# Optimization experiments

Hardware: AMD Instinct MI355X
Metric: run time of the kernel (lower is better)

The kernel has to match this reference:

```python
import jax, jax.numpy as jnp
import numpy as np

N = 50000          # nodes
E_RAND = 800000    # random edges (avg degree 16); self-loops appended per PyG GATConv default
IN = 128
HID = 32
HEADS = 4
OUT = 32
NEG_SLOPE = 0.2    # PyG GATConv default LeakyReLU slope


def setup_inputs() -> dict:
    key = jax.random.key(0)
    ks = jax.random.split(key, 8)
    x = jax.random.normal(ks[0], (N, IN), dtype=jnp.float32)
    src = jax.random.randint(ks[1], (E_RAND,), 0, N)
    dst = jax.random.randint(ks[2], (E_RAND,), 0, N)
    loops = jnp.arange(N)
    src = jnp.concatenate([src, loops])  # [E] with self-loops
    dst = jnp.concatenate([dst, loops])
    inp = {"x": x, "src": src, "dst": dst}
    layer_dims = [(IN, HID), (HID * HEADS, HID), (HID * HEADS, OUT)]
    for l, (din, c) in enumerate(layer_dims):
        k1, k2, k3 = jax.random.split(ks[3 + l], 3)
        s = 1.0 / np.sqrt(din)
        inp[f"W{l}"] = jax.random.uniform(k1, (HEADS * c, din), jnp.float32, -s, s)
        inp[f"asrc{l}"] = jax.random.uniform(k2, (HEADS, c), jnp.float32, -s, s)
        inp[f"adst{l}"] = jax.random.uniform(k3, (HEADS, c), jnp.float32, -s, s)
        inp[f"b{l}"] = jnp.zeros((HEADS * c,), jnp.float32)
    return inp


def _gat_conv(x, src, dst, W, a_src, a_dst, b):
    H, C = a_src.shape
    h = (x @ W.T).reshape(-1, H, C)                     # [N, H, C]
    al_s = jnp.einsum('nhc,hc->nh', h, a_src)           # node-level src score
    al_d = jnp.einsum('nhc,hc->nh', h, a_dst)           # node-level dst score
    e = jax.nn.leaky_relu(al_s[src] + al_d[dst], NEG_SLOPE)  # [E, H]
    # segment softmax over edges sharing the same destination node
    e_max = jax.ops.segment_max(e, dst, num_segments=N)
    e = jnp.exp(e - e_max[dst])
    denom = jax.ops.segment_sum(e, dst, num_segments=N)
    alpha = e / (denom[dst] + 1e-16)                    # [E, H]
    out = jax.ops.segment_sum(alpha[:, :, None] * h[src], dst, num_segments=N)  # [N, H, C]
    return out.reshape(-1, H * C) + b


def reference(x, src, dst, W0, asrc0, adst0, b0, W1, asrc1, adst1, b1, W2, asrc2, adst2, b2):
    params = [(W0, asrc0, adst0, b0), (W1, asrc1, adst1, b1), (W2, asrc2, adst2, b2)]
    h = x
    for i, (W, a_s, a_d, b) in enumerate(params):
        h = _gat_conv(h, src, dst, W, a_s, a_d, b)
        if i != len(params) - 1:
            h = jax.nn.elu(h)  # dropout p=0.5 is identity in eval mode
    return h
```

## Files before the change

### kernel.cpp

```cpp
#include <hip/hip_runtime.h>
#include <stdint.h>

typedef unsigned short ushort_t;
typedef unsigned int uint32;

typedef __attribute__((ext_vector_type(8))) short short8;
typedef __attribute__((ext_vector_type(4))) float floatx4;

#define NEG_SLOPE 0.2f

__device__ __forceinline__ ushort_t f2bf(float f) {
    union { float f; uint32 u; } v; v.f = f;
    uint32 u = v.u;
    uint32 r = (u + 0x7fffu + ((u >> 16) & 1u)) >> 16;
    return (ushort_t)r;
}
__device__ __forceinline__ float2 bf2x(uint32 u) {
    union { uint32 u; float f; } a, b;
    a.u = u << 16; b.u = u & 0xffff0000u;
    float2 r; r.x = a.f; r.y = b.f; return r;
}

__global__ void k_sniff(const uint32* __restrict__ x, int* __restrict__ flag) {
    __shared__ int sh[256];
    int t = threadIdx.x;
    int c = 0;
    for (int i = t; i < 1024; i += 256) {
        uint32 h = x[i] & 0xFFFFu;
        uint32 e = (h >> 7) & 0xFFu;
        if (h == 0u || (e >= 100u && e <= 140u)) c++;
    }
    sh[t] = c; __syncthreads();
    for (int off = 128; off >= 1; off >>= 1) {
        if (t < off) sh[t] += sh[t + off];
        __syncthreads();
    }
    if (t == 0) flag[0] = (sh[0] >= 512) ? 1 : 0;
}

__device__ __forceinline__ void gemm_body(int bid, int tid,
                                          const void* __restrict__ actv,
                                          const ushort_t* __restrict__ W,
                                          ushort_t* __restrict__ hb,
                                          float* __restrict__ als,
                                          float* __restrict__ ald,
                                          const ushort_t* __restrict__ asrcp,
                                          const ushort_t* __restrict__ adstp,
                                          int N, int layer0,
                                          const int* __restrict__ flag) {
    int wid = tid >> 6, lane = tid & 63;
    int n0 = (bid * 4 + wid) * 16;
    int mrow = lane & 15, quad = lane >> 4;
    int n = n0 + mrow;
    bool isf32 = (layer0 && !flag[0]);
    short8 a[4];
    if (n < N) {
        if (isf32) {
            const float* ar = (const float*)actv + (size_t)n * 128 + quad * 8;
            #pragma unroll
            for (int kt = 0; kt < 4; kt++) {
                float4 fa = *(const float4*)(ar + kt * 32);
                float4 fb = *(const float4*)(ar + kt * 32 + 4);
                short8 v;
                v[0] = (short)f2bf(fa.x); v[1] = (short)f2bf(fa.y);
                v[2] = (short)f2bf(fa.z); v[3] = (short)f2bf(fa.w);
                v[4] = (short)f2bf(fb.x); v[5] = (short)f2bf(fb.y);
                v[6] = (short)f2bf(fb.z); v[7] = (short)f2bf(fb.w);
                a[kt] = v;
            }
        } else {
            const ushort_t* ar = (const ushort_t*)actv + (size_t)n * 128 + quad * 8;
            #pragma unroll
            for (int kt = 0; kt < 4; kt++) a[kt] = *(const short8*)(ar + kt * 32);
        }
    } else {
        #pragma unroll
        for (int kt = 0; kt < 4; kt++) { short8 z = {0,0,0,0,0,0,0,0}; a[kt] = z; }
    }
    float ps[4], pd[4];
    #pragma unroll
    for (int t = 0; t < 8; t++) {
        if ((t & 1) == 0) {
            #pragma unroll
            for (int r = 0; r < 4; r++) { ps[r] = 0.f; pd[r] = 0.f; }
        }
        const ushort_t* wr = W + (size_t)(t * 16 + mrow) * 128 + quad * 8;
        floatx4 acc = {0.f, 0.f, 0.f, 0.f};
        #pragma unroll
        for (int kt = 0; kt < 4; kt++) {
            short8 b = *(const short8*)(wr + kt * 32);
            acc = __builtin_amdgcn_mfma_f32_16x16x32_bf16(a[kt], b, acc, 0, 0, 0);
        }
        int col = t * 16 + mrow;
        union { uint32 u; float f; } cs, cd;
        cs.u = ((uint32)asrcp[col]) << 16;
        cd.u = ((uint32)adstp[col]) << 16;
        #pragma unroll
        for (int r = 0; r < 4; r++) {
            int rn = n0 + quad * 4 + r;
            if (rn < N) hb[(size_t)rn * 128 + col] = f2bf(acc[r]);
            ps[r] += acc[r] * cs.f;
            pd[r] += acc[r] * cd.f;
        }
        if (t & 1) {
            #pragma unroll
            for (int off = 1; off <= 8; off <<= 1) {
                #pragma unroll
                for (int r = 0; r < 4; r++) {
                    ps[r] += __shfl_xor(ps[r], off);
                    pd[r] += __shfl_xor(pd[r], off);
                }
            }
            int h = t >> 1;
            if (mrow < 8) {
                int r = mrow & 3;
                float vs = r == 0 ? ps[0] : r == 1 ? ps[1] : r == 2 ? ps[2] : ps[3];
                float vd = r == 0 ? pd[0] : r == 1 ? pd[1] : r == 2 ? pd[2] : pd[3];
                int rn = n0 + quad * 4 + r;
                if (rn < N) {
                    float* dp = (mrow < 4) ? als : ald;
                    dp[(size_t)rn * 4 + h] = (mrow < 4) ? vs : vd;
                }
            }
        }
    }
}

__global__ __launch_bounds__(256) void k_gemm(const void* __restrict__ actv,
                                              const ushort_t* __restrict__ W,
                                              ushort_t* __restrict__ hb,
                                              float* __restrict__ als,
                                              float* __restrict__ ald,
                                              const ushort_t* __restrict__ asrcp,
                                              const ushort_t* __restrict__ adstp,
                                              int N, const int* __restrict__ flag) {
    gemm_body(blockIdx.x, threadIdx.x, actv, W, hb, als, ald, asrcp, adstp, N, 0, flag);
}

__global__ void k_f1(const void* W0, const void* W1, const void* W2,
                     const void* s0, const void* s1, const void* s2,
                     const void* a0, const void* a1, const void* a2,
                     const void* b0, const void* b1, const void* b2,
                     ushort_t* __restrict__ pblk, const int* __restrict__ flag,
                     const int* __restrict__ dst, int* __restrict__ cnt,
                     int* __restrict__ rank, int E) {
    if (blockIdx.x < 197) {
        int i = blockIdx.x * 256 + threadIdx.x;
        if (i >= 50304) return;
        const void* src; int off;
        if (i < 49152) {
            int seg = i / 16384; off = i % 16384;
            src = seg == 0 ? W0 : seg == 1 ? W1 : W2;
        } else if (i < 49536) {
            int j = i - 49152; int seg = j / 128; off = j % 128;
            src = seg == 0 ? s0 : seg == 1 ? s1 : s2;
        } else if (i < 49920) {
            int j = i - 49536; int seg = j / 128; off = j % 128;
            src = seg == 0 ? a0 : seg == 1 ? a1 : a2;
        } else {
            int j = i - 49920; int seg = j / 128; off = j % 128;
            src = seg == 0 ? b0 : seg == 1 ? b1 : b2;
        }
        if (flag[0]) pblk[i] = ((const ushort_t*)src)[off];
        else         pblk[i] = f2bf(((const float*)src)[off]);
    } else {
        int e0 = ((blockIdx.x - 197) * 256 + threadIdx.x) * 4;
        if (e0 + 3 < E) {
            int4 d4 = *(const int4*)(dst + e0);
            int r0 = atomicAdd(&cnt[d4.x], 1);
            int r1 = atomicAdd(&cnt[d4.y], 1);
            int r2 = atomicAdd(&cnt[d4.z], 1);
            int r3 = atomicAdd(&cnt[d4.w], 1);
            int4 r4 = {r0, r1, r2, r3};
            *(int4*)(rank + e0) = r4;
        } else {
            for (int e = e0; e < E; e++) rank[e] = atomicAdd(&cnt[dst[e]], 1);
        }
    }
}

__global__ __launch_bounds__(256) void k_f2(const int* __restrict__ cnt, int* __restrict__ ro,
                                            int* __restrict__ bsum, int n, int nb,
                                            const void* __restrict__ actv,
                                            const ushort_t* __restrict__ W,
                                            ushort_t* __restrict__ hb,
                                            float* __restrict__ als, float* __restrict__ ald,
                                            const ushort_t* __restrict__ asrcp,
                                            const ushort_t* __restrict__ adstp,
                                            int N, const int* __restrict__ flag) {
    if ((int)blockIdx.x < nb) {
        __shared__ int sd[256];
        int t = threadIdx.x;
        int base = blockIdx.x * 1024 + t * 4;
        int v0 = (base + 0 < n) ? cnt[base + 0] : 0;
        int v1 = (base + 1 < n) ? cnt[base + 1] : 0;
        int v2 = (base + 2 < n) ? cnt[base + 2] : 0;
        int v3 = (base + 3 < n) ? cnt[base + 3] : 0;
        int s = v0 + v1 + v2 + v3;
        sd[t] = s; __syncthreads();
        for (int off = 1; off < 256; off <<= 1) {
            int x = 0;
            if (t >= off) x = sd[t - off];
            __syncthreads();
            sd[t] += x;
            __syncthreads();
        }
        int run = sd[t] - s;
        run += v0; if (base + 0 < n) ro[base + 1] = run;
        run += v1; if (base + 1 < n) ro[base + 2] = run;
        run += v2; if (base + 2 < n) ro[base + 3] = run;
        run += v3; if (base + 3 < n) ro[base + 4] = run;
        if (t == 255) bsum[blockIdx.x] = sd[255];
    } else {
        gemm_body(blockIdx.x - nb, threadIdx.x, actv, W, hb, als, ald, asrcp, adstp, N, 1, flag);
    }
}

__global__ void k_scan_bc(int* __restrict__ ro, const int* __restrict__ bsum,
                          int n, int nb) {
    __shared__ int pre[256];
    int t = threadIdx.x;
    if (t == 0) {
        int acc = 0;
        for (int b = 0; b < nb; b++) { pre[b] = acc; acc += bsum[b]; }
    }
    __syncthreads();
    int i = blockIdx.x * 256 + t;
    if (i == 0) ro[0] = 0;
    if (i < n) ro[i + 1] += pre[i >> 10];
}

__global__ void k_scatter(const int* __restrict__ src, const int* __restrict__ dst,
                          const int* __restrict__ ro, const int* __restrict__ rank,
                          ushort_t* __restrict__ ssrc, int E) {
    int e0 = (blockIdx.x * 256 + threadIdx.x) * 4;
    if (e0 + 3 < E) {
        int4 d4 = *(const int4*)(dst + e0);
        int4 s4 = *(const int4*)(src + e0);
        int4 r4 = *(const int4*)(rank + e0);
        ssrc[ro[d4.x] + r4.x] = (ushort_t)s4.x;
        ssrc[ro[d4.y] + r4.y] = (ushort_t)s4.y;
        ssrc[ro[d4.z] + r4.z] = (ushort_t)s4.z;
        ssrc[ro[d4.w] + r4.w] = (ushort_t)s4.w;
    } else {
        for (int e = e0; e < E; e++) ssrc[ro[dst[e]] + rank[e]] = (ushort_t)src[e];
    }
}

__global__ __launch_bounds__(64) void k_agg(const int* __restrict__ ro,
                                            const ushort_t* __restrict__ ssrc,
                                            const ushort_t* __restrict__ hb,
                                            const float* __restrict__ als,
                                            const float* __restrict__ ald_,
                                            const ushort_t* __restrict__ bias,
                                            void* __restrict__ outp, int N, int apply_elu,
                                            int is_final, const int* __restrict__ flag) {
    int n = blockIdx.x;
    int lane = threadIdx.x;
    int r0 = ro[n], r1 = ro[n + 1];
    floatx4 ad = *(const floatx4*)(ald_ + (size_t)n * 4);
    const char* alsb = (const char*)als;

    __shared__ __align__(16) float wsm[256];
    __shared__ int osm[64];
    float a0 = 0.f, a1 = 0.f;
    float d0 = 0.f, d1 = 0.f, d2 = 0.f, d3 = 0.f;
    int hd = lane >> 4;
    int laneb = lane << 2;
    for (int base = r0; base < r1; base += 64) {
        int i = base + lane;
        if (i < r1) {
            int s = ssrc[i];
            floatx4 as = *(const floatx4*)(alsb + (s << 4));
            float t0 = as.x + ad.x; float w0 = __expf(fmaxf(t0, NEG_SLOPE * t0)); d0 += w0;
            float t1 = as.y + ad.y; float w1 = __expf(fmaxf(t1, NEG_SLOPE * t1)); d1 += w1;
            float t2 = as.z + ad.z; float w2 = __expf(fmaxf(t2, NEG_SLOPE * t2)); d2 += w2;
            float t3 = as.w + ad.w; float w3 = __expf(fmaxf(t3, NEG_SLOPE * t3)); d3 += w3;
            osm[lane] = s << 8;
            floatx4 w4 = {w0, w1, w2, w3};
            *(floatx4*)(wsm + lane * 4) = w4;
        }
        __builtin_amdgcn_wave_barrier();
        int cend = min(64, r1 - base);
        #pragma unroll 4
        for (int j = 0; j < cend; j++) {
            float wj = wsm[j * 4 + hd];
            uint32 h2 = *(const uint32*)((const char*)hb + (uint32)(osm[j] + laneb));
            float2 p = bf2x(h2);
            a0 += wj * p.x;
            a1 += wj * p.y;
        }
        __builtin_amdgcn_wave_barrier();
    }
    #pragma unroll
    for (int off = 32; off >= 1; off >>= 1) {
        d0 += __shfl_xor(d0, off); d1 += __shfl_xor(d1, off);
        d2 += __shfl_xor(d2, off); d3 += __shfl_xor(d3, off);
    }
    float den = (hd == 0 ? d0 : hd == 1 ? d1 : hd == 2 ? d2 : d3) + 1e-16f;
    float inv = 1.0f / den;
    int c0 = lane * 2;
    float2 bv = bf2x(*(const uint32*)(bias + c0));
    float o0 = a0 * inv + bv.x;
    float o1 = a1 * inv + bv.y;
    if (apply_elu) {
        o0 = o0 > 0.f ? o0 : expm1f(o0);
        o1 = o1 > 0.f ? o1 : expm1f(o1);
    }
    if (is_final && !flag[0]) {
        float2 o; o.x = o0; o.y = o1;
        *(float2*)((float*)outp + (size_t)n * 128 + c0) = o;
    } else {
        uint32 pack = (uint32)f2bf(o0) | ((uint32)f2bf(o1) << 16);
        *(uint32*)((ushort_t*)outp + (size_t)n * 128 + c0) = pack;
    }
}

extern "C" void kernel_launch(void* const* d_in, const int* in_sizes, int n_in,
                              void* d_out, int out_size, void* d_ws, size_t ws_size,
                              hipStream_t stream) {
    const void* x = d_in[0];
    const int* src = (const int*)d_in[1];
    const int* dst = (const int*)d_in[2];
    const int N = in_sizes[0] / 128;
    const int E = in_sizes[1];

    char* p = (char*)d_ws;
    auto alloc = [&](size_t bytes) { char* r = p; p += (bytes + 255) & ~(size_t)255; return r; };
    int*      flag  = (int*)alloc(256);
    int*      bsum  = (int*)alloc(256 * 4);
    int*      ro    = (int*)alloc((size_t)(N + 1) * 4);
    ushort_t* ssrc  = (ushort_t*)alloc((size_t)E * 2);
    ushort_t* hb    = (ushort_t*)alloc((size_t)N * 128 * 2);
    float*    als   = (float*)alloc((size_t)N * 4 * 4);
    float*    ald   = (float*)alloc((size_t)N * 4 * 4);
    ushort_t* xact  = (ushort_t*)alloc((size_t)N * 128 * 2);
    ushort_t* pblk  = (ushort_t*)alloc((size_t)50304 * 2);

    int* cnt  = (int*)ssrc;
    int* rank = (int*)xact;

    int g256e4 = (E + 1023) / 1024;
    int g256n = (N + 255) / 256;
    int nb = (N + 1023) / 1024;
    int gg = (N + 63) / 64;

    k_sniff<<<1, 256, 0, stream>>>((const uint32*)x, flag);
    hipMemsetAsync(cnt, 0, (size_t)N * 4, stream);
    k_f1<<<197 + g256e4, 256, 0, stream>>>(
        d_in[3], d_in[7], d_in[11],
        d_in[4], d_in[8], d_in[12],
        d_in[5], d_in[9], d_in[13],
        d_in[6], d_in[10], d_in[14],
        pblk, flag, dst, cnt, rank, E);
    k_f2<<<nb + gg, 256, 0, stream>>>(cnt, ro, bsum, N, nb,
        x, pblk, hb, als, ald, pblk + 49152, pblk + 49536, N, flag);
    k_scan_bc<<<g256n, 256, 0, stream>>>(ro, bsum, N, nb);
    k_scatter<<<g256e4, 256, 0, stream>>>(src, dst, ro, rank, ssrc, E);

    for (int l = 0; l < 3; l++) {
        const ushort_t* As = pblk + 49152 + l * 128;
        const ushort_t* Ad = pblk + 49536 + l * 128;
        const ushort_t* Bc = pblk + 49920 + l * 128;
        void* outp = (l == 2) ? d_out : (void*)xact;
        if (l > 0) {
            const ushort_t* Wc = pblk + (size_t)l * 16384;
            k_gemm<<<gg, 256, 0, stream>>>(xact, Wc, hb, als, ald, As, Ad, N, flag);
        }
        k_agg<<<N, 64, 0, stream>>>(ro, ssrc, hb, als, ald, Bc, outp, N, l < 2 ? 1 : 0,
                                    l == 2 ? 1 : 0, flag);
    }
}
```

Measured before the change: 333.4 us.

## Fuse scatter with layer-0 GEMM, pack two nodes per agg block, dual accumulators

Moves the block-level scan into its own kernel, then fuses the CSR scatter with the layer-0 GEMM in one launch, in place of fusing the scan with the GEMM. The aggregation kernel now runs two nodes per 128-thread block, one wave each, to halve the block count. Its inner loop is unrolled by two with independent accumulators to expose more memory-level parallelism. An unused k_f3 variant is added, and the scan and GEMM are no longer overlapped.

After: 358.6 us. +7.5%, slower.

```diff
diff --git a/kernel.cpp b/kernel.cpp
--- a/kernel.cpp
+++ b/kernel.cpp
@@ -179,8 +179,49 @@
     }
 }
 
-__global__ __launch_bounds__(256) void k_f2(const int* __restrict__ cnt, int* __restrict__ ro,
-                                            int* __restrict__ bsum, int n, int nb,
+__global__ void k_scan_a(const int* __restrict__ cnt, int* __restrict__ ro,
+                         int* __restrict__ bsum, int n) {
+    __shared__ int sd[256];
+    int t = threadIdx.x;
+    int base = blockIdx.x * 1024 + t * 4;
+    int v0 = (base + 0 < n) ? cnt[base + 0] : 0;
+    int v1 = (base + 1 < n) ? cnt[base + 1] : 0;
+    int v2 = (base + 2 < n) ? cnt[base + 2] : 0;
+    int v3 = (base + 3 < n) ? cnt[base + 3] : 0;
+    int s = v0 + v1 + v2 + v3;
+    sd[t] = s; __syncthreads();
+    for (int off = 1; off < 256; off <<= 1) {
+        int x = 0;
+        if (t >= off) x = sd[t - off];
+        __syncthreads();
+        sd[t] += x;
+        __syncthreads();
+    }
+    int run = sd[t] - s;
+    run += v0; if (base + 0 < n) ro[base + 1] = run;
+    run += v1; if (base + 1 < n) ro[base + 2] = run;
+    run += v2; if (base + 2 < n) ro[base + 3] = run;
+    run += v3; if (base + 3 < n) ro[base + 4] = run;
+    if (t == 255) bsum[blockIdx.x] = sd[255];
+}
+
+__global__ void k_scan_bc(int* __restrict__ ro, const int* __restrict__ bsum,
+                          int n, int nb) {
+    __shared__ int pre[256];
+    int t = threadIdx.x;
+    if (t == 0) {
+        int acc = 0;
+        for (int b = 0; b < nb; b++) { pre[b] = acc; acc += bsum[b]; }
+    }
+    __syncthreads();
+    int i = blockIdx.x * 256 + t;
+    if (i == 0) ro[0] = 0;
+    if (i < n) ro[i + 1] += pre[i >> 10];
+}
+
+__global__ __launch_bounds__(256) void k_f3(const int* __restrict__ src, const int* __restrict__ dst,
+                                            const int* __restrict__ ro, const int* __restrict__ rank,
+                                            ushort_t* __restrict__ ssrc, int E, int ns,
                                             const void* __restrict__ actv,
                                             const ushort_t* __restrict__ W,
                                             ushort_t* __restrict__ hb,
@@ -188,82 +229,72 @@
                                             const ushort_t* __restrict__ asrcp,
                                             const ushort_t* __restrict__ adstp,
                                             int N, const int* __restrict__ flag) {
-    if ((int)blockIdx.x < nb) {
-        __shared__ int sd[256];
-        int t = threadIdx.x;
-        int base = blockIdx.x * 1024 + t * 4;
-        int v0 = (base + 0 < n) ? cnt[base + 0] : 0;
-        int v1 = (base + 1 < n) ? cnt[base + 1] : 0;
-        int v2 = (base + 2 < n) ? cnt[base + 2] : 0;
-        int v3 = (base + 3 < n) ? cnt[base + 3] : 0;
-        int s = v0 + v1 + v2 + v3;
-        sd[t] = s; __syncthreads();
-        for (int off = 1; off < 256; off <<= 1) {
-            int x = 0;
-            if (t >= off) x = sd[t - off];
-            __syncthreads();
-            sd[t] += x;
-            __syncthreads();
-        }
-        int run = sd[t] - s;
-        run += v0; if (base + 0 < n) ro[base + 1] = run;
-        run += v1; if (base + 1 < n) ro[base + 2] = run;
-        run += v2; if (base + 2 < n) ro[base + 3] = run;
-        run += v3; if (base + 3 < n) ro[base + 4] = run;
-        if (t == 255) bsum[blockIdx.x] = sd[255];
+    if ((int)blockIdx.x < ns) {
+        int e0 = (blockIdx.x * 256 + threadIdx.x) * 4;
+        if (e0 + 3 < E) {
+            int4 d4 = *(const int4*)(dst + e0);
+            int4 s4 = *(const int4*)(src + e0);
+            int4 r4 = *(const int4*)(rank + e0);
+            ssrc[ro[d4.x] + r4.x] = (ushort_t)s4.x;
+            ssrc[ro[d4.y] + r4.y] = (ushort_t)s4.y;
+            ssrc[ro[d4.z] + r4.z] = (ushort_t)s4.z;
+            ssrc[ro[d4.w] + r4.w] = (ushort_t)s4.w;
+        } else {
+            for (int e = e0; e < E; e++) ssrc[ro[dst[e]] + rank[e]] = (ushort_t)src[e];
+        }
     } else {
-        gemm_body(blockIdx.x - nb, threadIdx.x, actv, W, hb, als, ald, asrcp, adstp, N, 1, flag);
-    }
-}
-
-__global__ void k_scan_bc(int* __restrict__ ro, const int* __restrict__ bsum,
-                          int n, int nb) {
-    __shared__ int pre[256];
-    int t = threadIdx.x;
-    if (t == 0) {
-        int acc = 0;
-        for (int b = 0; b < nb; b++) { pre[b] = acc; acc += bsum[b]; }
-    }
-    __syncthreads();
-    int i = blockIdx.x * 256 + t;
-    if (i == 0) ro[0] = 0;
-    if (i < n) ro[i + 1] += pre[i >> 10];
-}
-
-__global__ void k_scatter(const int* __restrict__ src, const int* __restrict__ dst,
-                          const int* __restrict__ ro, const int* __restrict__ rank,
-                          ushort_t* __restrict__ ssrc, int E) {
-    int e0 = (blockIdx.x * 256 + threadIdx.x) * 4;
-    if (e0 + 3 < E) {
-        int4 d4 = *(const int4*)(dst + e0);
-        int4 s4 = *(const int4*)(src + e0);
-        int4 r4 = *(const int4*)(rank + e0);
-        ssrc[ro[d4.x] + r4.x] = (ushort_t)s4.x;
-        ssrc[ro[d4.y] + r4.y] = (ushort_t)s4.y;
-        ssrc[ro[d4.z] + r4.z] = (ushort_t)s4.z;
-        ssrc[ro[d4.w] + r4.w] = (ushort_t)s4.w;
+        gemm_body(blockIdx.x - ns, threadIdx.x, actv, W, hb, als, ald, asrcp, adstp, N, 0 , flag);
+    }
+}
+
+__global__ __launch_bounds__(256) void k_f3_l0(const int* __restrict__ src, const int* __restrict__ dst,
+                                               const int* __restrict__ ro, const int* __restrict__ rank,
+                                               ushort_t* __restrict__ ssrc, int E, int ns,
+                                               const void* __restrict__ actv,
+                                               const ushort_t* __restrict__ W,
+                                               ushort_t* __restrict__ hb,
+                                               float* __restrict__ als, float* __restrict__ ald,
+                                               const ushort_t* __restrict__ asrcp,
+                                               const ushort_t* __restrict__ adstp,
+                                               int N, const int* __restrict__ flag) {
+    if ((int)blockIdx.x < ns) {
+        int e0 = (blockIdx.x * 256 + threadIdx.x) * 4;
+        if (e0 + 3 < E) {
+            int4 d4 = *(const int4*)(dst + e0);
+            int4 s4 = *(const int4*)(src + e0);
+            int4 r4 = *(const int4*)(rank + e0);
+            ssrc[ro[d4.x] + r4.x] = (ushort_t)s4.x;
+            ssrc[ro[d4.y] + r4.y] = (ushort_t)s4.y;
+            ssrc[ro[d4.z] + r4.z] = (ushort_t)s4.z;
+            ssrc[ro[d4.w] + r4.w] = (ushort_t)s4.w;
+        } else {
+            for (int e = e0; e < E; e++) ssrc[ro[dst[e]] + rank[e]] = (ushort_t)src[e];
+        }
     } else {
-        for (int e = e0; e < E; e++) ssrc[ro[dst[e]] + rank[e]] = (ushort_t)src[e];
-    }
-}
-
-__global__ __launch_bounds__(64) void k_agg(const int* __restrict__ ro,
-                                            const ushort_t* __restrict__ ssrc,
-                                            const ushort_t* __restrict__ hb,
-                                            const float* __restrict__ als,
-                                            const float* __restrict__ ald_,
-                                            const ushort_t* __restrict__ bias,
-                                            void* __restrict__ outp, int N, int apply_elu,
-                                            int is_final, const int* __restrict__ flag) {
-    int n = blockIdx.x;
-    int lane = threadIdx.x;
+        gemm_body(blockIdx.x - ns, threadIdx.x, actv, W, hb, als, ald, asrcp, adstp, N, 1, flag);
+    }
+}
+
+__global__ __launch_bounds__(128) void k_agg(const int* __restrict__ ro,
+                                             const ushort_t* __restrict__ ssrc,
+                                             const ushort_t* __restrict__ hb,
+                                             const float* __restrict__ als,
+                                             const float* __restrict__ ald_,
+                                             const ushort_t* __restrict__ bias,
+                                             void* __restrict__ outp, int N, int apply_elu,
+                                             int is_final, const int* __restrict__ flag) {
+    __shared__ __align__(16) float wsm_all[2][256];
+    __shared__ int osm_all[2][64];
+    int wv = threadIdx.x >> 6, lane = threadIdx.x & 63;
+    int n = blockIdx.x * 2 + wv;
+    if (n >= N) return;
+    float* wsm = wsm_all[wv];
+    int* osm = osm_all[wv];
     int r0 = ro[n], r1 = ro[n + 1];
     floatx4 ad = *(const floatx4*)(ald_ + (size_t)n * 4);
     const char* alsb = (const char*)als;
 
-    __shared__ __align__(16) float wsm[256];
-    __shared__ int osm[64];
-    float a0 = 0.f, a1 = 0.f;
+    float a0 = 0.f, a1 = 0.f, b0 = 0.f, b1 = 0.f;
     float d0 = 0.f, d1 = 0.f, d2 = 0.f, d3 = 0.f;
     int hd = lane >> 4;
     int laneb = lane << 2;
@@ -282,16 +313,25 @@
         }
         __builtin_amdgcn_wave_barrier();
         int cend = min(64, r1 - base);
-        #pragma unroll 4
-        for (int j = 0; j < cend; j++) {
-            float wj = wsm[j * 4 + hd];
-            uint32 h2 = *(const uint32*)((const char*)hb + (uint32)(osm[j] + laneb));
-            float2 p = bf2x(h2);
-            a0 += wj * p.x;
-            a1 += wj * p.y;
+        int j = 0;
+        for (; j + 2 <= cend; j += 2) {
+            float wj0 = wsm[j * 4 + hd];
+            float wj1 = wsm[j * 4 + 4 + hd];
+            uint32 h0 = *(const uint32*)((const char*)hb + (uint32)(osm[j] + laneb));
+            uint32 h1 = *(const uint32*)((const char*)hb + (uint32)(osm[j + 1] + laneb));
+            float2 p0 = bf2x(h0), p1 = bf2x(h1);
+            a0 += wj0 * p0.x; a1 += wj0 * p0.y;
+            b0 += wj1 * p1.x; b1 += wj1 * p1.y;
+        }
+        if (j < cend) {
+            float wj0 = wsm[j * 4 + hd];
+            uint32 h0 = *(const uint32*)((const char*)hb + (uint32)(osm[j] + laneb));
+            float2 p0 = bf2x(h0);
+            a0 += wj0 * p0.x; a1 += wj0 * p0.y;
         }
         __builtin_amdgcn_wave_barrier();
     }
+    a0 += b0; a1 += b1;
     #pragma unroll
     for (int off = 32; off >= 1; off >>= 1) {
         d0 += __shfl_xor(d0, off); d1 += __shfl_xor(d1, off);
@@ -353,11 +393,12 @@
         d_in[5], d_in[9], d_in[13],
         d_in[6], d_in[10], d_in[14],
         pblk, flag, dst, cnt, rank, E);
-    k_f2<<<nb + gg, 256, 0, stream>>>(cnt, ro, bsum, N, nb,
+    k_scan_a<<<nb, 256, 0, stream>>>(cnt, ro, bsum, N);
+    k_scan_bc<<<g256n, 256, 0, stream>>>(ro, bsum, N, nb);
+    k_f3_l0<<<g256e4 + gg, 256, 0, stream>>>(src, dst, ro, rank, ssrc, E, g256e4,
         x, pblk, hb, als, ald, pblk + 49152, pblk + 49536, N, flag);
-    k_scan_bc<<<g256n, 256, 0, stream>>>(ro, bsum, N, nb);
-    k_scatter<<<g256e4, 256, 0, stream>>>(src, dst, ro, rank, ssrc, E);
-
+
+    int ga = (N + 1) / 2;
     for (int l = 0; l < 3; l++) {
         const ushort_t* As = pblk + 49152 + l * 128;
         const ushort_t* Ad = pblk + 49536 + l * 128;
@@ -367,7 +408,7 @@
             const ushort_t* Wc = pblk + (size_t)l * 16384;
             k_gemm<<<gg, 256, 0, stream>>>(xact, Wc, hb, als, ald, As, Ad, N, flag);
         }
-        k_agg<<<N, 64, 0, stream>>>(ro, ssrc, hb, als, ald, Bc, outp, N, l < 2 ? 1 : 0,
-                                    l == 2 ? 1 : 0, flag);
-    }
-}
+        k_agg<<<ga, 128, 0, stream>>>(ro, ssrc, hb, als, ald, Bc, outp, N, l < 2 ? 1 : 0,
+                                      l == 2 ? 1 : 0, flag);
+    }
+}
```

## Split aggregation per node into two head-pair blocks with two edges per iteration

Applied to the files above, without the earlier changes.

Each destination node is now handled by two 64-thread blocks, one per pair of heads. Within a block, each half-wave processes a different edge, so each iteration consumes two edges, and two accumulator sets add memory-level parallelism. The half-wave partial sums are combined with a cross-lane shuffle, and only the lower half writes output. The aim is more latency-hiding parallelism on the gather loop. The cost is doubling the block count, recomputing the source-index and score loads in both blocks, and a zero-padding entry for odd edge counts.

After: 358.2 us. 7.4% more time.

```diff
diff --git a/kernel.cpp b/kernel.cpp
--- a/kernel.cpp
+++ b/kernel.cpp
@@ -255,64 +255,86 @@
                                             const ushort_t* __restrict__ bias,
                                             void* __restrict__ outp, int N, int apply_elu,
                                             int is_final, const int* __restrict__ flag) {
-    int n = blockIdx.x;
+    int bid = blockIdx.x;
+    int n = bid >> 1;
+    int hp = bid & 1;
     int lane = threadIdx.x;
     int r0 = ro[n], r1 = ro[n + 1];
-    floatx4 ad = *(const floatx4*)(ald_ + (size_t)n * 4);
-    const char* alsb = (const char*)als;
-
-    __shared__ __align__(16) float wsm[256];
+    float2 adp = *(const float2*)(ald_ + (size_t)n * 4 + hp * 2);
+    const char* alsb = (const char*)als + hp * 8;
+
+    __shared__ __align__(8) float wsm[128];
     __shared__ int osm[64];
-    float a0 = 0.f, a1 = 0.f;
-    float d0 = 0.f, d1 = 0.f, d2 = 0.f, d3 = 0.f;
-    int hd = lane >> 4;
-    int laneb = lane << 2;
+    float a0 = 0.f, a1 = 0.f, b0 = 0.f, b1 = 0.f;
+    float d0 = 0.f, d1 = 0.f;
+    int eh = lane >> 5;
+    int l5 = lane & 31;
+    int hd2 = l5 >> 4;
+    int chb = hp * 128 + l5 * 4;
+
     for (int base = r0; base < r1; base += 64) {
         int i = base + lane;
+        int cend = min(64, r1 - base);
         if (i < r1) {
             int s = ssrc[i];
-            floatx4 as = *(const floatx4*)(alsb + (s << 4));
-            float t0 = as.x + ad.x; float w0 = __expf(fmaxf(t0, NEG_SLOPE * t0)); d0 += w0;
-            float t1 = as.y + ad.y; float w1 = __expf(fmaxf(t1, NEG_SLOPE * t1)); d1 += w1;
-            float t2 = as.z + ad.z; float w2 = __expf(fmaxf(t2, NEG_SLOPE * t2)); d2 += w2;
-            float t3 = as.w + ad.w; float w3 = __expf(fmaxf(t3, NEG_SLOPE * t3)); d3 += w3;
+            float2 as = *(const float2*)(alsb + (s << 4));
+            float t0 = as.x + adp.x; float w0 = __expf(fmaxf(t0, NEG_SLOPE * t0)); d0 += w0;
+            float t1 = as.y + adp.y; float w1 = __expf(fmaxf(t1, NEG_SLOPE * t1)); d1 += w1;
             osm[lane] = s << 8;
-            floatx4 w4 = {w0, w1, w2, w3};
-            *(floatx4*)(wsm + lane * 4) = w4;
+            float2 w2v; w2v.x = w0; w2v.y = w1;
+            *(float2*)(wsm + lane * 2) = w2v;
+        } else if (lane == cend) {
+            osm[lane] = 0;
+            float2 z; z.x = 0.f; z.y = 0.f;
+            *(float2*)(wsm + lane * 2) = z;
         }
         __builtin_amdgcn_wave_barrier();
-        int cend = min(64, r1 - base);
-        #pragma unroll 4
-        for (int j = 0; j < cend; j++) {
-            float wj = wsm[j * 4 + hd];
-            uint32 h2 = *(const uint32*)((const char*)hb + (uint32)(osm[j] + laneb));
-            float2 p = bf2x(h2);
-            a0 += wj * p.x;
-            a1 += wj * p.y;
+        int trips = (cend + 1) >> 1;
+        int j2 = 0;
+        for (; j2 + 2 <= trips; j2 += 2) {
+            int e0i = j2 * 2 + eh;
+            int e1i = j2 * 2 + 2 + eh;
+            float wj0 = wsm[e0i * 2 + hd2];
+            float wj1 = wsm[e1i * 2 + hd2];
+            uint32 h0 = *(const uint32*)((const char*)hb + (uint32)(osm[e0i] + chb));
+            uint32 h1 = *(const uint32*)((const char*)hb + (uint32)(osm[e1i] + chb));
+            float2 p0 = bf2x(h0), p1 = bf2x(h1);
+            a0 += wj0 * p0.x; a1 += wj0 * p0.y;
+            b0 += wj1 * p1.x; b1 += wj1 * p1.y;
+        }
+        if (j2 < trips) {
+            int e0i = j2 * 2 + eh;
+            float wj0 = wsm[e0i * 2 + hd2];
+            uint32 h0 = *(const uint32*)((const char*)hb + (uint32)(osm[e0i] + chb));
+            float2 p0 = bf2x(h0);
+            a0 += wj0 * p0.x; a1 += wj0 * p0.y;
         }
         __builtin_amdgcn_wave_barrier();
     }
+    a0 += b0; a1 += b1;
+    a0 += __shfl_xor(a0, 32); a1 += __shfl_xor(a1, 32);
     #pragma unroll
     for (int off = 32; off >= 1; off >>= 1) {
-        d0 += __shfl_xor(d0, off); d1 += __shfl_xor(d1, off);
-        d2 += __shfl_xor(d2, off); d3 += __shfl_xor(d3, off);
-    }
-    float den = (hd == 0 ? d0 : hd == 1 ? d1 : hd == 2 ? d2 : d3) + 1e-16f;
-    float inv = 1.0f / den;
-    int c0 = lane * 2;
-    float2 bv = bf2x(*(const uint32*)(bias + c0));
-    float o0 = a0 * inv + bv.x;
-    float o1 = a1 * inv + bv.y;
-    if (apply_elu) {
-        o0 = o0 > 0.f ? o0 : expm1f(o0);
-        o1 = o1 > 0.f ? o1 : expm1f(o1);
-    }
-    if (is_final && !flag[0]) {
-        float2 o; o.x = o0; o.y = o1;
-        *(float2*)((float*)outp + (size_t)n * 128 + c0) = o;
-    } else {
-        uint32 pack = (uint32)f2bf(o0) | ((uint32)f2bf(o1) << 16);
-        *(uint32*)((ushort_t*)outp + (size_t)n * 128 + c0) = pack;
+        d0 += __shfl_xor(d0, off);
+        d1 += __shfl_xor(d1, off);
+    }
+    if (eh == 0) {
+        float den = (hd2 == 0 ? d0 : d1) + 1e-16f;
+        float inv = 1.0f / den;
+        float2 bv = bf2x(*(const uint32*)((const char*)bias + chb));
+        float o0 = a0 * inv + bv.x;
+        float o1 = a1 * inv + bv.y;
+        if (apply_elu) {
+            o0 = o0 > 0.f ? o0 : expm1f(o0);
+            o1 = o1 > 0.f ? o1 : expm1f(o1);
+        }
+        if (is_final && !flag[0]) {
+            float2 o; o.x = o0; o.y = o1;
+            *(float2*)((char*)outp + (size_t)n * 512 + chb * 2) = o;
+        } else {
+            uint32 pack = (uint32)f2bf(o0) | ((uint32)f2bf(o1) << 16);
+            *(uint32*)((char*)outp + (size_t)n * 256 + chb) = pack;
+        }
     }
 }
 
@@ -367,7 +389,7 @@
             const ushort_t* Wc = pblk + (size_t)l * 16384;
             k_gemm<<<gg, 256, 0, stream>>>(xact, Wc, hb, als, ald, As, Ad, N, flag);
         }
-        k_agg<<<N, 64, 0, stream>>>(ro, ssrc, hb, als, ald, Bc, outp, N, l < 2 ? 1 : 0,
-                                    l == 2 ? 1 : 0, flag);
-    }
-}
+        k_agg<<<N * 2, 64, 0, stream>>>(ro, ssrc, hb, als, ald, Bc, outp, N, l < 2 ? 1 : 0,
+                                        l == 2 ? 1 : 0, flag);
+    }
+}
```
